# Optimization experiments

Measured on AMD Instinct MI355X. Metric: run time of the kernel, lower is better.

The kernel has to match this reference:

```python
import jax, jax.numpy as jnp
import numpy as np

B, D, H, O, E = 16384, 1024, 512, 256, 8


def setup_inputs() -> dict:
    key = jax.random.key(0)
    ks = jax.random.split(key, 8)
    s = lambda k, shape, fan: (jax.random.normal(k, shape, jnp.float32) / np.sqrt(fan).astype(np.float32))
    z = lambda shape: jnp.zeros(shape, jnp.float32)
    return {
        "x": jax.random.normal(ks[0], (B, D), jnp.float32),
        # gating network: D -> 256 -> 128 -> E
        "gw1": s(ks[1], (D, 256), D), "gb1": z((256,)),
        "gw2": s(ks[2], (256, 128), 256), "gb2": z((128,)),
        "gw3": s(ks[3], (128, E), 128), "gb3": z((E,)),
        # experts, batched over expert dim E: D -> H -> H -> O
        "ew1": s(ks[4], (E, D, H), D), "eb1": z((E, H)),
        "ew2": s(ks[5], (E, H, H), H), "eb2": z((E, H)),
        "ew3": s(ks[6], (E, H, O), H), "eb3": z((E, O)),
    }


def reference(x, gw1, gb1, gw2, gb2, gw3, gb3, ew1, eb1, ew2, eb2, ew3, eb3):
    # Gating network (dropout is identity in eval mode)
    g = jax.nn.relu(x @ gw1 + gb1)
    g = jax.nn.relu(g @ gw2 + gb2)
    gates = jax.nn.softmax(g @ gw3 + gb3, axis=1)  # [B, E]
    # All experts run on every token: batched small MLPs over expert axis e
    h = jax.nn.relu(jnp.einsum('bd,edh->ebh', x, ew1) + eb1[:, None, :])   # [E, B, H]
    h = jax.nn.relu(jnp.einsum('ebh,ehk->ebk', h, ew2) + eb2[:, None, :])  # [E, B, H]
    eo = jnp.einsum('ebh,eho->ebo', h, ew3) + eb3[:, None, :]              # [E, B, O]
    # gate-weighted sum over experts
    out = jnp.einsum('ebo,be->bo', eo, gates)  # [B, O]
    return out
```

## Files before the change

kernel.cpp:

```cpp
#include <hip/hip_runtime.h>
#include <hip/hip_bf16.h>

typedef __hip_bfloat16 bf16;
typedef __attribute__((ext_vector_type(8))) __bf16 bf16x8;
typedef __attribute__((ext_vector_type(4))) float f32x4;

#define B_ 16384
#define D_ 1024
#define H_ 512
#define O_ 256
#define E_ 8
#define BC_ 8192

#define GLDS(src, dst) __builtin_amdgcn_global_load_lds( \
    (const __attribute__((address_space(1))) void*)(src), \
    (__attribute__((address_space(3))) void*)(dst), 16, 0, 0)

__global__ void detect_k(const unsigned short* __restrict__ x, int* __restrict__ flag) {
    __shared__ int s;
    if (threadIdx.x == 0) s = 0;
    __syncthreads();
    int big = 0;
    for (int i = threadIdx.x; i < 2048; i += 256)
        if (((x[i] >> 7) & 0xFF) >= 150) big = 1;
    if (big) atomicOr(&s, 1);
    __syncthreads();
    if (threadIdx.x == 0) *flag = s;
}

__global__ void cvt_k(const void* __restrict__ src, bf16* __restrict__ dst,
                      const int* __restrict__ flag, long n) {
    const int f = *flag;
    long i = (long)blockIdx.x * blockDim.x + threadIdx.x;
    const long stride = (long)gridDim.x * blockDim.x;
    if (f) {
        const float* s = (const float*)src;
        for (; i < n; i += stride) dst[i] = __float2bfloat16(s[i]);
    } else {
        const bf16* s = (const bf16*)src;
        for (; i < n; i += stride) dst[i] = s[i];
    }
}

__global__ void transpose_k(const void* __restrict__ in, bf16* __restrict__ out,
                            const int* __restrict__ flag, int R, int C) {
    __shared__ bf16 t[32][33];
    const int f = *flag;
    const long zo = (long)blockIdx.z * R * C;
    const int x = blockIdx.x * 32 + threadIdx.x;
    const int y0 = blockIdx.y * 32;
    const float* inf = (const float*)in;
    const bf16* inb = (const bf16*)in;
#pragma unroll
    for (int i = 0; i < 4; i++) {
        int r = y0 + threadIdx.y + i * 8;
        long idx = zo + (long)r * C + x;
        t[threadIdx.y + i * 8][threadIdx.x] =
            f ? __float2bfloat16(inf[idx]) : inb[idx];
    }
    __syncthreads();
    const int xr = blockIdx.y * 32 + threadIdx.x;
#pragma unroll
    for (int i = 0; i < 4; i++) {
        int c = blockIdx.x * 32 + threadIdx.y + i * 8;
        out[zo + (long)c * R + xr] = t[threadIdx.x][threadIdx.y + i * 8];
    }
}

__global__ void gate3_softmax_k(const bf16* __restrict__ g2,
                                const bf16* __restrict__ gw3,
                                const bf16* __restrict__ gb3,
                                float* __restrict__ gates) {
    __shared__ float w[128 * 8];
    __shared__ float bsh[8];
    const int tid = threadIdx.x;
    for (int i = tid; i < 1024; i += 256) w[i] = __bfloat162float(gw3[i]);
    if (tid < 8) bsh[tid] = __bfloat162float(gb3[tid]);
    __syncthreads();

    const long row = (long)blockIdx.x * 256 + tid;
    float acc[8];
#pragma unroll
    for (int o = 0; o < 8; o++) acc[o] = bsh[o];

    const bf16x8* rp8 = (const bf16x8*)(g2 + row * 128);
#pragma unroll 4
    for (int c8 = 0; c8 < 16; c8++) {
        bf16x8 v8 = rp8[c8];
#pragma unroll
        for (int jj = 0; jj < 8; jj++) {
            float v = (float)v8[jj];
            int k = c8 * 8 + jj;
#pragma unroll
            for (int o = 0; o < 8; o++) acc[o] += v * w[k * 8 + o];
        }
    }
    float m = acc[0];
#pragma unroll
    for (int o = 1; o < 8; o++) m = fmaxf(m, acc[o]);
    float s = 0.f;
#pragma unroll
    for (int o = 0; o < 8; o++) { acc[o] = __expf(acc[o] - m); s += acc[o]; }
    const float inv = 1.f / s;
#pragma unroll
    for (int o = 0; o < 8; o++) gates[row * 8 + o] = acc[o] * inv;
}

template <int MODE>
__global__ __launch_bounds__(256, 4)
void gemm_bt(const bf16* __restrict__ A, const bf16* __restrict__ Bt,
             const bf16* __restrict__ bias, const float* __restrict__ gates,
             void* __restrict__ Cout, const bf16* __restrict__ eb3,
             const int* __restrict__ oflag,
             int lda, int ldb, int ldo, int K,
             long a_z, long b_z, long bias_z, long out_z,
             int e_gate, int k_per_e, long a_e, long b_e, long row0) {
    __shared__ __attribute__((aligned(16))) bf16 As[128 * 32];
    __shared__ __attribute__((aligned(16))) bf16 Bs[128 * 32];

    const int tid  = threadIdx.x;
    const int lane = tid & 63;
    const int quad = lane >> 4;
    const int l15  = lane & 15;
    const int wid  = tid >> 6;
    const int wr   = (wid >> 1) << 6;
    const int wc   = (wid & 1) << 6;
    const int z    = blockIdx.z;
    const long m0  = (long)blockIdx.y << 7;
    const long n0  = (long)blockIdx.x << 7;

    const bf16* Az = A + (long)z * a_z;
    const bf16* Bz = Bt + (long)z * b_z;

    f32x4 acc[4][4];
#pragma unroll
    for (int i = 0; i < 4; i++)
#pragma unroll
        for (int j = 0; j < 4; j++) acc[i][j] = (f32x4){0.f, 0.f, 0.f, 0.f};

    const int erow = tid >> 2;
    const int ecol = (tid & 3) << 3;

    const int n_e   = k_per_e ? (K / k_per_e) : 1;
    const int inner = (k_per_e ? k_per_e : K) >> 5;

    for (int e = 0; e < n_e; e++) {
        const bf16* Ae = Az + (long)e * a_e;
        const bf16* Be = Bz + (long)e * b_e;
        for (int kti = 0; kti < inner; kti++) {
            const int kk = kti << 5;
#pragma unroll
            for (int i = 0; i < 2; i++) {
                const int r = (i << 6) + erow;
                GLDS(Ae + (m0 + r) * lda + (kk + ecol), As + r * 32 + ecol);
            }
#pragma unroll
            for (int i = 0; i < 2; i++) {
                const int r = (i << 6) + erow;
                GLDS(Be + (n0 + r) * ldb + (kk + ecol), Bs + r * 32 + ecol);
            }
            __syncthreads();
            bf16x8 af[4], bfr[4];
#pragma unroll
            for (int i = 0; i < 4; i++)
                af[i] = *(const bf16x8*)(As + (wr + i * 16 + l15) * 32 + (quad << 3));
#pragma unroll
            for (int j = 0; j < 4; j++)
                bfr[j] = *(const bf16x8*)(Bs + (wc + j * 16 + l15) * 32 + (quad << 3));
#pragma unroll
            for (int i = 0; i < 4; i++)
#pragma unroll
                for (int j = 0; j < 4; j++)
                    acc[i][j] = __builtin_amdgcn_mfma_f32_16x16x32_bf16(
                        af[i], bfr[j], acc[i][j], 0, 0, 0);
            __syncthreads();
        }
    }

    const int eg = (e_gate >= 0) ? e_gate : z;

    if constexpr (MODE == 0 || MODE == 1) {
        bf16* C = (bf16*)Cout + (long)z * out_z;
        const bf16* bb = bias + (long)z * bias_z;
        float gv[4][4];
        if constexpr (MODE == 1) {
#pragma unroll
            for (int i = 0; i < 4; i++)
#pragma unroll
                for (int rg = 0; rg < 4; rg++)
                    gv[i][rg] = gates[(row0 + m0 + wr + i * 16 + quad * 4 + rg) * 8 + eg];
        }
#pragma unroll
        for (int j = 0; j < 4; j++) {
            const int c = (int)n0 + wc + j * 16 + l15;
            const float bv = __bfloat162float(bb[c]);
#pragma unroll
            for (int i = 0; i < 4; i++) {
#pragma unroll
                for (int rg = 0; rg < 4; rg++) {
                    const long r = m0 + wr + i * 16 + quad * 4 + rg;
                    float v = fmaxf(acc[i][j][rg] + bv, 0.f);
                    if constexpr (MODE == 1) v *= gv[i][rg];
                    C[r * ldo + c] = __float2bfloat16(v);
                }
            }
        }
    } else if constexpr (MODE == 2) {
        float* C = (float*)Cout;
#pragma unroll
        for (int i = 0; i < 4; i++) {
#pragma unroll
            for (int rg = 0; rg < 4; rg++) {
                const long r = m0 + wr + i * 16 + quad * 4 + rg;
                const float g = gates[(row0 + r) * 8 + eg];
#pragma unroll
                for (int j = 0; j < 4; j++) {
                    const int c = (int)n0 + wc + j * 16 + l15;
                    const float b3 = __bfloat162float(eb3[eg * O_ + c]);
                    C[r * ldo + c] += acc[i][j][rg] + g * b3;
                }
            }
        }
    } else {
        float* C = (float*)Cout + (long)z * out_z;
        const int e0 = z * 2;
        float b30[4], b31[4];
#pragma unroll
        for (int j = 0; j < 4; j++) {
            const int c = (int)n0 + wc + j * 16 + l15;
            b30[j] = __bfloat162float(eb3[e0 * O_ + c]);
            b31[j] = __bfloat162float(eb3[(e0 + 1) * O_ + c]);
        }
#pragma unroll
        for (int i = 0; i < 4; i++) {
#pragma unroll
            for (int rg = 0; rg < 4; rg++) {
                const long r = m0 + wr + i * 16 + quad * 4 + rg;
                const float g0 = gates[(row0 + r) * 8 + e0];
                const float g1 = gates[(row0 + r) * 8 + e0 + 1];
#pragma unroll
                for (int j = 0; j < 4; j++) {
                    const int c = (int)n0 + wc + j * 16 + l15;
                    C[(row0 + r) * ldo + c] =
                        acc[i][j][rg] + g0 * b30[j] + g1 * b31[j];
                }
            }
        }
    }
}

__global__ void zero_f32_k(float* __restrict__ p) {
    p[(long)blockIdx.x * 256 + threadIdx.x] = 0.f;
}
__global__ void out_cvt_k(const float* __restrict__ in, void* __restrict__ out,
                          const int* __restrict__ flag) {
    const long i = (long)blockIdx.x * 256 + threadIdx.x;
    if (*flag) ((float*)out)[i] = in[i];
    else       ((bf16*)out)[i] = __float2bfloat16(in[i]);
}
__global__ void reduce4_k(const float* __restrict__ p, void* __restrict__ out,
                          const int* __restrict__ flag) {
    const long n = (long)B_ * O_;
    const long i = ((long)blockIdx.x * 256 + threadIdx.x) * 4;
    float4 a = *(const float4*)(p + i);
    float4 b = *(const float4*)(p + n + i);
    float4 c = *(const float4*)(p + 2 * n + i);
    float4 d = *(const float4*)(p + 3 * n + i);
    float4 s = {a.x + b.x + c.x + d.x, a.y + b.y + c.y + d.y,
                a.z + b.z + c.z + d.z, a.w + b.w + c.w + d.w};
    if (*flag) {
        *(float4*)((float*)out + i) = s;
    } else {
        bf16* o = (bf16*)out + i;
        o[0] = __float2bfloat16(s.x); o[1] = __float2bfloat16(s.y);
        o[2] = __float2bfloat16(s.z); o[3] = __float2bfloat16(s.w);
    }
}

extern "C" void kernel_launch(void* const* d_in, const int* in_sizes, int n_in,
                              void* d_out, int out_size, void* d_ws, size_t ws_size,
                              hipStream_t stream) {
    (void)in_sizes; (void)n_in; (void)out_size;
    const void* x   = d_in[0];
    const void* gw1 = d_in[1];
    const void* gb1 = d_in[2];
    const void* gw2 = d_in[3];
    const void* gb2 = d_in[4];
    const void* gw3 = d_in[5];
    const void* gb3 = d_in[6];
    const void* ew1 = d_in[7];
    const void* eb1 = d_in[8];
    const void* ew2 = d_in[9];
    const void* eb2 = d_in[10];
    const void* ew3 = d_in[11];
    const void* eb3 = d_in[12];

    char* ws = (char*)d_ws;
    size_t off = 0;
    auto alloc = [&](size_t n) { char* p = ws + off; off += (n + 255) & ~(size_t)255; return p; };

    int*  flag  = (int*)alloc(256);
    bf16* xc    = (bf16*)alloc((size_t)B_ * D_ * 2);
    bf16* gw1t  = (bf16*)alloc((size_t)256 * 1024 * 2);
    bf16* gw2t  = (bf16*)alloc((size_t)128 * 256 * 2);
    bf16* ew1t  = (bf16*)alloc((size_t)E_ * H_ * D_ * 2);
    bf16* ew2t  = (bf16*)alloc((size_t)E_ * H_ * H_ * 2);
    bf16* ew3t  = (bf16*)alloc((size_t)E_ * O_ * H_ * 2);
    bf16* gb1c  = (bf16*)alloc(256 * 2);
    bf16* gb2c  = (bf16*)alloc(128 * 2);
    bf16* gw3c  = (bf16*)alloc(1024 * 2);
    bf16* gb3c  = (bf16*)alloc(8 * 2);
    bf16* eb1c  = (bf16*)alloc((size_t)E_ * H_ * 2);
    bf16* eb2c  = (bf16*)alloc((size_t)E_ * H_ * 2);
    bf16* eb3c  = (bf16*)alloc((size_t)E_ * O_ * 2);
    bf16* g1    = (bf16*)alloc((size_t)B_ * 256 * 2);
    bf16* g2b   = (bf16*)alloc((size_t)B_ * 128 * 2);
    float* gates = (float*)alloc((size_t)B_ * 8 * 4);

    const size_t small = off;
    const size_t needA = small + 2ull * ((size_t)E_ * BC_ * H_ * 2 + 256)
                               + (4ull * B_ * O_ * 4 + 256) + 4096;
    const bool pathA = ws_size >= needA;

    detect_k<<<1, 256, 0, stream>>>((const unsigned short*)x, flag);

    cvt_k<<<4096, 256, 0, stream>>>(x, xc, flag, (long)B_ * D_);
    cvt_k<<<1, 256, 0, stream>>>(gb1, gb1c, flag, 256);
    cvt_k<<<1, 256, 0, stream>>>(gb2, gb2c, flag, 128);
    cvt_k<<<4, 256, 0, stream>>>(gw3, gw3c, flag, 1024);
    cvt_k<<<1, 256, 0, stream>>>(gb3, gb3c, flag, 8);
    cvt_k<<<16, 256, 0, stream>>>(eb1, eb1c, flag, (long)E_ * H_);
    cvt_k<<<16, 256, 0, stream>>>(eb2, eb2c, flag, (long)E_ * H_);
    cvt_k<<<8, 256, 0, stream>>>(eb3, eb3c, flag, (long)E_ * O_);

    transpose_k<<<dim3(256 / 32, 1024 / 32, 1), dim3(32, 8), 0, stream>>>(gw1, gw1t, flag, 1024, 256);
    transpose_k<<<dim3(128 / 32, 256 / 32, 1), dim3(32, 8), 0, stream>>>(gw2, gw2t, flag, 256, 128);
    transpose_k<<<dim3(H_ / 32, D_ / 32, E_), dim3(32, 8), 0, stream>>>(ew1, ew1t, flag, D_, H_);
    transpose_k<<<dim3(H_ / 32, H_ / 32, E_), dim3(32, 8), 0, stream>>>(ew2, ew2t, flag, H_, H_);
    transpose_k<<<dim3(O_ / 32, H_ / 32, E_), dim3(32, 8), 0, stream>>>(ew3, ew3t, flag, H_, O_);

    gemm_bt<0><<<dim3(2, 128, 1), 256, 0, stream>>>(
        xc, gw1t, gb1c, nullptr, g1, nullptr, nullptr,
        1024, 1024, 256, 1024, 0, 0, 0, 0, 0, 0, 0, 0, 0);
    gemm_bt<0><<<dim3(1, 128, 1), 256, 0, stream>>>(
        g1, gw2t, gb2c, nullptr, g2b, nullptr, nullptr,
        256, 256, 128, 256, 0, 0, 0, 0, 0, 0, 0, 0, 0);
    gate3_softmax_k<<<dim3(B_ / 256), 256, 0, stream>>>(g2b, gw3c, gb3c, gates);

    if (pathA) {
        bf16* h1c = (bf16*)alloc((size_t)E_ * BC_ * H_ * 2);
        bf16* h2c = (bf16*)alloc((size_t)E_ * BC_ * H_ * 2);
        float* parts = (float*)alloc(4ull * B_ * O_ * 4);
        for (int ci = 0; ci < B_ / BC_; ci++) {
            const long rb = (long)ci * BC_;
            gemm_bt<0><<<dim3(4, BC_ / 128, 8), 256, 0, stream>>>(
                xc + rb * D_, ew1t, eb1c, nullptr, h1c, nullptr, nullptr,
                D_, D_, H_, D_,
                0, (long)H_ * D_, H_, (long)BC_ * H_, 0, 0, 0, 0, 0);
            gemm_bt<1><<<dim3(4, BC_ / 128, 8), 256, 0, stream>>>(
                h1c, ew2t, eb2c, gates, h2c, nullptr, nullptr,
                H_, H_, H_, H_,
                (long)BC_ * H_, (long)H_ * H_, H_, (long)BC_ * H_, -1, 0, 0, 0, rb);
            gemm_bt<5><<<dim3(2, BC_ / 128, 4), 256, 0, stream>>>(
                h2c, ew3t, nullptr, gates, parts, eb3c, nullptr,
                H_, H_, O_, 1024,
                2L * BC_ * H_, 2L * O_ * H_, 0, (long)B_ * O_,
                2 , 512, (long)BC_ * H_, (long)O_ * H_, rb);
        }
        reduce4_k<<<dim3(B_ * O_ / 1024), 256, 0, stream>>>(parts, d_out, flag);
    } else {
        bf16* h1s = (bf16*)alloc((size_t)B_ * H_ * 2);
        bf16* h2s = (bf16*)alloc((size_t)B_ * H_ * 2);
        float* oacc = (float*)alloc((size_t)B_ * O_ * 4);
        zero_f32_k<<<dim3(B_ * O_ / 256), 256, 0, stream>>>(oacc);
        for (int e = 0; e < E_; e++) {
            gemm_bt<0><<<dim3(4, 128, 1), 256, 0, stream>>>(
                xc, ew1t + (size_t)e * H_ * D_, eb1c + (size_t)e * H_, nullptr, h1s, nullptr, nullptr,
                1024, 1024, 512, 1024, 0, 0, 0, 0, 0, 0, 0, 0, 0);
            gemm_bt<1><<<dim3(4, 128, 1), 256, 0, stream>>>(
                h1s, ew2t + (size_t)e * H_ * H_, eb2c + (size_t)e * H_, gates, h2s, nullptr, nullptr,
                512, 512, 512, 512, 0, 0, 0, 0, e, 0, 0, 0, 0);
            gemm_bt<2><<<dim3(2, 128, 1), 256, 0, stream>>>(
                h2s, ew3t + (size_t)e * O_ * H_, nullptr, gates, oacc, eb3c, nullptr,
                512, 512, 256, 512, 0, 0, 0, 0, e, 0, 0, 0, 0);
        }
        out_cvt_k<<<dim3(B_ * O_ / 256), 256, 0, stream>>>(oacc, d_out, flag);
    }
}
```

Baseline: 587.8 us.

## Replace expert GEMMs with 256x256-tile 8-wave pipelined MFMA kernel

Adds a gemm256 kernel with 256x256 output tiles, 512 threads, double-buffered LDS filled by global_load_lds with XOR swizzle, interleaved staging and MFMA phases, and workgroup ID remapping. It replaces the three expert GEMMs on the chunked path. Expert-2 output and the ew3 transpose now use an interleaved [B, E*H] layout, so layer 3 runs per expert into 8 partial buffers. Those partials are summed per chunk by a new reduce8 kernel. The aim is higher MFMA utilisation and more data reuse, at the cost of more register pressure, more partial-buffer traffic, and per-chunk reduce launches.

Result: no change. 580.2 us (-1.3%).

```diff
diff --git a/kernel.cpp b/kernel.cpp
--- a/kernel.cpp
+++ b/kernel.cpp
@@ -12,9 +12,15 @@
 #define E_ 8
 #define BC_ 8192
 
+static_assert(B_ % BC_ == 0, "chunking");
+
 #define GLDS(src, dst) __builtin_amdgcn_global_load_lds( \
     (const __attribute__((address_space(1))) void*)(src), \
     (__attribute__((address_space(3))) void*)(dst), 16, 0, 0)
+
+#define BAR()   asm volatile("s_barrier" ::: "memory")
+#define LGKM0() do { asm volatile("s_waitcnt lgkmcnt(0)" ::: "memory"); \
+                     __builtin_amdgcn_sched_barrier(0); } while (0)
 
 __global__ void detect_k(const unsigned short* __restrict__ x, int* __restrict__ flag) {
     __shared__ int s;
@@ -43,10 +49,11 @@
 }
 
 __global__ void transpose_k(const void* __restrict__ in, bf16* __restrict__ out,
-                            const int* __restrict__ flag, int R, int C) {
+                            const int* __restrict__ flag, int R, int C,
+                            long z_out, long c_stride) {
     __shared__ bf16 t[32][33];
     const int f = *flag;
-    const long zo = (long)blockIdx.z * R * C;
+    const long zi = (long)blockIdx.z * R * C;
     const int x = blockIdx.x * 32 + threadIdx.x;
     const int y0 = blockIdx.y * 32;
     const float* inf = (const float*)in;
@@ -54,16 +61,17 @@
 #pragma unroll
     for (int i = 0; i < 4; i++) {
         int r = y0 + threadIdx.y + i * 8;
-        long idx = zo + (long)r * C + x;
+        long idx = zi + (long)r * C + x;
         t[threadIdx.y + i * 8][threadIdx.x] =
             f ? __float2bfloat16(inf[idx]) : inb[idx];
     }
     __syncthreads();
     const int xr = blockIdx.y * 32 + threadIdx.x;
+    const long zo = (long)blockIdx.z * z_out;
 #pragma unroll
     for (int i = 0; i < 4; i++) {
         int c = blockIdx.x * 32 + threadIdx.y + i * 8;
-        out[zo + (long)c * R + xr] = t[threadIdx.x][threadIdx.y + i * 8];
+        out[zo + (long)c * c_stride + xr] = t[threadIdx.x][threadIdx.y + i * 8];
     }
 }
 
@@ -221,28 +229,189 @@
                 }
             }
         }
+    }
+}
+
+template <int MODE>
+__global__ __launch_bounds__(512, 2)
+void gemm256(const bf16* __restrict__ A, const bf16* __restrict__ Bt,
+             const bf16* __restrict__ bias, const float* __restrict__ gates,
+             void* __restrict__ Cout, const bf16* __restrict__ eb3,
+             int lda, int ldb, int ldo, int K,
+             long a_z, long b_z, long bias_z, long out_z, long row0) {
+    __shared__ __attribute__((aligned(16))) bf16 lds[2][2][256 * 64];
+
+    int bx = blockIdx.x, by = blockIdx.y;
+    {
+        const int gx = gridDim.x;
+        const int nwg = gx * gridDim.y;
+        if ((nwg & 7) == 0) {
+            int lin = bx + gx * by;
+            lin = (lin & 7) * (nwg >> 3) + (lin >> 3);
+            bx = lin % gx; by = lin / gx;
+        }
+    }
+
+    const int tid  = threadIdx.x;
+    const int lane = tid & 63;
+    const int quad = lane >> 4;
+    const int l15  = lane & 15;
+    const int w    = tid >> 6;
+    const int wm   = w >> 2;
+    const int wn   = w & 3;
+    const int z    = blockIdx.z;
+    const long m0  = (long)by << 8;
+    const long n0  = (long)bx << 8;
+
+    const bf16* __restrict__ Az = A + z * a_z;
+    const bf16* __restrict__ Bz = Bt + z * b_z;
+
+    f32x4 acc[8][4];
+#pragma unroll
+    for (int i = 0; i < 8; ++i)
+#pragma unroll
+        for (int j = 0; j < 4; ++j) acc[i][j] = (f32x4){0.f, 0.f, 0.f, 0.f};
+
+    bf16x8 af[4][2], bv[2][2];
+
+    auto stage = [&](int buf, int mat, int half, int kt) {
+        const bf16* __restrict__ G = mat ? Bz : Az;
+        const int ld = mat ? ldb : lda;
+        const long p0 = mat ? n0 : m0;
+#pragma unroll
+        for (int l = 0; l < 2; ++l) {
+            const int ci = (w << 1) | l;
+            const int rb = mat ? ((ci >> 2) << 6) + (half << 5) + ((ci & 3) << 3)
+                               : ((ci >> 3) << 7) + (half << 6) + ((ci & 7) << 3);
+            const int row = rb + (lane >> 3);
+            const int cb  = ((lane & 7) << 4) ^ ((row & 4) << 3);
+            GLDS(G + (p0 + row) * ld + kt * 64 + (cb >> 1),
+                 &lds[buf][mat][rb * 64]);
+        }
+    };
+    auto ldaf = [&](int buf, int qm) {
+#pragma unroll
+        for (int i = 0; i < 4; ++i) {
+            const int r = (wm << 7) + (qm << 6) + (i << 4) + l15;
+            const char* p = (const char*)&lds[buf][0][r * 64];
+            const int sw = (r & 4) << 3;
+#pragma unroll
+            for (int s = 0; s < 2; ++s)
+                af[i][s] = *(const bf16x8*)(p + (((s << 6) + (quad << 4)) ^ sw));
+        }
+    };
+    auto ldbf = [&](int buf, int qn) {
+#pragma unroll
+        for (int j = 0; j < 2; ++j) {
+            const int r = (wn << 6) + (qn << 5) + (j << 4) + l15;
+            const char* p = (const char*)&lds[buf][1][r * 64];
+            const int sw = (r & 4) << 3;
+#pragma unroll
+            for (int s = 0; s < 2; ++s)
+                bv[j][s] = *(const bf16x8*)(p + (((s << 6) + (quad << 4)) ^ sw));
+        }
+    };
+    auto mmac = [&](int qm, int qn) {
+#pragma unroll
+        for (int i = 0; i < 4; ++i)
+#pragma unroll
+            for (int j = 0; j < 2; ++j)
+#pragma unroll
+                for (int s = 0; s < 2; ++s)
+                    acc[(qm << 2) + i][(qn << 1) + j] =
+                        __builtin_amdgcn_mfma_f32_16x16x32_bf16(
+                            af[i][s], bv[j][s], acc[(qm << 2) + i][(qn << 1) + j],
+                            0, 0, 0);
+    };
+
+    const int nt = K >> 6;
+
+    stage(0, 0, 0, 0); stage(0, 0, 1, 0); stage(0, 1, 0, 0); stage(0, 1, 1, 0);
+    stage(1, 0, 0, 1); stage(1, 1, 0, 1);
+    asm volatile("s_waitcnt vmcnt(4)" ::: "memory");
+    BAR();
+
+    const int hi = nt >> 1;
+    for (int it = 0; it < hi; ++it) {
+        const int t1k = 2 * it + 1, t2k = 2 * it + 2, t3k = 2 * it + 3;
+        const bool do2 = t2k < nt, do3 = t3k < nt;
+        ldaf(0, 0); ldbf(0, 0); stage(1, 0, 1, t1k);
+        BAR(); LGKM0();
+        __builtin_amdgcn_s_setprio(1); mmac(0, 0); __builtin_amdgcn_s_setprio(0);
+        BAR();
+        ldbf(0, 1); stage(1, 1, 1, t1k);
+        BAR(); LGKM0();
+        __builtin_amdgcn_s_setprio(1); mmac(0, 1); __builtin_amdgcn_s_setprio(0);
+        BAR();
+        ldaf(0, 1); ldbf(0, 0); if (do2) stage(0, 0, 0, t2k);
+        BAR(); LGKM0();
+        __builtin_amdgcn_s_setprio(1); mmac(1, 0); __builtin_amdgcn_s_setprio(0);
+        BAR();
+        ldbf(0, 1); if (do2) stage(0, 1, 0, t2k);
+        BAR(); LGKM0();
+        __builtin_amdgcn_s_setprio(1); mmac(1, 1); __builtin_amdgcn_s_setprio(0);
+        if (do2) { asm volatile("s_waitcnt vmcnt(4)" ::: "memory"); }
+        else     { asm volatile("s_waitcnt vmcnt(0)" ::: "memory"); }
+        BAR();
+        ldaf(1, 0); ldbf(1, 0); if (do2) stage(0, 0, 1, t2k);
+        BAR(); LGKM0();
+        __builtin_amdgcn_s_setprio(1); mmac(0, 0); __builtin_amdgcn_s_setprio(0);
+        BAR();
+        ldbf(1, 1); if (do2) stage(0, 1, 1, t2k);
+        BAR(); LGKM0();
+        __builtin_amdgcn_s_setprio(1); mmac(0, 1); __builtin_amdgcn_s_setprio(0);
+        BAR();
+        ldaf(1, 1); ldbf(1, 0); if (do3) stage(1, 0, 0, t3k);
+        BAR(); LGKM0();
+        __builtin_amdgcn_s_setprio(1); mmac(1, 0); __builtin_amdgcn_s_setprio(0);
+        BAR();
+        ldbf(1, 1); if (do3) stage(1, 1, 0, t3k);
+        BAR(); LGKM0();
+        __builtin_amdgcn_s_setprio(1); mmac(1, 1); __builtin_amdgcn_s_setprio(0);
+        if (do3) { asm volatile("s_waitcnt vmcnt(4)" ::: "memory"); }
+        else     { asm volatile("s_waitcnt vmcnt(0)" ::: "memory"); }
+        BAR();
+    }
+
+    if constexpr (MODE == 0 || MODE == 1) {
+        bf16* C = (bf16*)Cout + z * out_z;
+        const bf16* bb = bias + z * bias_z;
+        float bvv[4];
+#pragma unroll
+        for (int jg = 0; jg < 4; ++jg)
+            bvv[jg] = __bfloat162float(bb[(int)n0 + (wn << 6) + (jg << 4) + l15]);
+#pragma unroll
+        for (int ig = 0; ig < 8; ++ig) {
+#pragma unroll
+            for (int rg = 0; rg < 4; ++rg) {
+                const long r = m0 + (wm << 7) + (ig << 4) + (quad << 2) + rg;
+                float g = 1.f;
+                if constexpr (MODE == 1) g = gates[(row0 + r) * 8 + z];
+#pragma unroll
+                for (int jg = 0; jg < 4; ++jg) {
+                    const int c = (int)n0 + (wn << 6) + (jg << 4) + l15;
+                    float v = fmaxf(acc[ig][jg][rg] + bvv[jg], 0.f);
+                    if constexpr (MODE == 1) v *= g;
+                    C[r * ldo + c] = __float2bfloat16(v);
+                }
+            }
+        }
     } else {
-        float* C = (float*)Cout + (long)z * out_z;
-        const int e0 = z * 2;
-        float b30[4], b31[4];
-#pragma unroll
-        for (int j = 0; j < 4; j++) {
-            const int c = (int)n0 + wc + j * 16 + l15;
-            b30[j] = __bfloat162float(eb3[e0 * O_ + c]);
-            b31[j] = __bfloat162float(eb3[(e0 + 1) * O_ + c]);
-        }
-#pragma unroll
-        for (int i = 0; i < 4; i++) {
-#pragma unroll
-            for (int rg = 0; rg < 4; rg++) {
-                const long r = m0 + wr + i * 16 + quad * 4 + rg;
-                const float g0 = gates[(row0 + r) * 8 + e0];
-                const float g1 = gates[(row0 + r) * 8 + e0 + 1];
-#pragma unroll
-                for (int j = 0; j < 4; j++) {
-                    const int c = (int)n0 + wc + j * 16 + l15;
-                    C[(row0 + r) * ldo + c] =
-                        acc[i][j][rg] + g0 * b30[j] + g1 * b31[j];
+        float* C = (float*)Cout + z * out_z;
+        float b3v[4];
+#pragma unroll
+        for (int jg = 0; jg < 4; ++jg)
+            b3v[jg] = __bfloat162float(eb3[z * O_ + (int)n0 + (wn << 6) + (jg << 4) + l15]);
+#pragma unroll
+        for (int ig = 0; ig < 8; ++ig) {
+#pragma unroll
+            for (int rg = 0; rg < 4; ++rg) {
+                const long r = m0 + (wm << 7) + (ig << 4) + (quad << 2) + rg;
+                const float g = gates[(row0 + r) * 8 + z];
+#pragma unroll
+                for (int jg = 0; jg < 4; ++jg) {
+                    const int c = (int)n0 + (wn << 6) + (jg << 4) + l15;
+                    C[r * ldo + c] = acc[ig][jg][rg] + g * b3v[jg];
                 }
             }
         }
@@ -258,20 +427,20 @@
     if (*flag) ((float*)out)[i] = in[i];
     else       ((bf16*)out)[i] = __float2bfloat16(in[i]);
 }
-__global__ void reduce4_k(const float* __restrict__ p, void* __restrict__ out,
-                          const int* __restrict__ flag) {
-    const long n = (long)B_ * O_;
+__global__ void reduce8_k(const float* __restrict__ p, void* __restrict__ out,
+                          const int* __restrict__ flag, long off) {
+    const long n = (long)BC_ * O_;
     const long i = ((long)blockIdx.x * 256 + threadIdx.x) * 4;
-    float4 a = *(const float4*)(p + i);
-    float4 b = *(const float4*)(p + n + i);
-    float4 c = *(const float4*)(p + 2 * n + i);
-    float4 d = *(const float4*)(p + 3 * n + i);
-    float4 s = {a.x + b.x + c.x + d.x, a.y + b.y + c.y + d.y,
-                a.z + b.z + c.z + d.z, a.w + b.w + c.w + d.w};
+    float4 s = *(const float4*)(p + i);
+#pragma unroll
+    for (int zz = 1; zz < 8; ++zz) {
+        float4 a = *(const float4*)(p + (long)zz * n + i);
+        s.x += a.x; s.y += a.y; s.z += a.z; s.w += a.w;
+    }
     if (*flag) {
-        *(float4*)((float*)out + i) = s;
+        *(float4*)((float*)out + off + i) = s;
     } else {
-        bf16* o = (bf16*)out + i;
+        bf16* o = (bf16*)out + off + i;
         o[0] = __float2bfloat16(s.x); o[1] = __float2bfloat16(s.y);
         o[2] = __float2bfloat16(s.z); o[3] = __float2bfloat16(s.w);
     }
@@ -318,8 +487,9 @@
     float* gates = (float*)alloc((size_t)B_ * 8 * 4);
 
     const size_t small = off;
-    const size_t needA = small + 2ull * ((size_t)E_ * BC_ * H_ * 2 + 256)
-                               + (4ull * B_ * O_ * 4 + 256) + 4096;
+    const size_t needA = small + ((size_t)E_ * BC_ * H_ * 2 + 256)
+                               + ((size_t)BC_ * E_ * H_ * 2 + 256)
+                               + (8ull * BC_ * O_ * 4 + 256) + 4096;
     const bool pathA = ws_size >= needA;
 
     detect_k<<<1, 256, 0, stream>>>((const unsigned short*)x, flag);
@@ -333,11 +503,20 @@
     cvt_k<<<16, 256, 0, stream>>>(eb2, eb2c, flag, (long)E_ * H_);
     cvt_k<<<8, 256, 0, stream>>>(eb3, eb3c, flag, (long)E_ * O_);
 
-    transpose_k<<<dim3(256 / 32, 1024 / 32, 1), dim3(32, 8), 0, stream>>>(gw1, gw1t, flag, 1024, 256);
-    transpose_k<<<dim3(128 / 32, 256 / 32, 1), dim3(32, 8), 0, stream>>>(gw2, gw2t, flag, 256, 128);
-    transpose_k<<<dim3(H_ / 32, D_ / 32, E_), dim3(32, 8), 0, stream>>>(ew1, ew1t, flag, D_, H_);
-    transpose_k<<<dim3(H_ / 32, H_ / 32, E_), dim3(32, 8), 0, stream>>>(ew2, ew2t, flag, H_, H_);
-    transpose_k<<<dim3(O_ / 32, H_ / 32, E_), dim3(32, 8), 0, stream>>>(ew3, ew3t, flag, H_, O_);
+    transpose_k<<<dim3(256 / 32, 1024 / 32, 1), dim3(32, 8), 0, stream>>>(
+        gw1, gw1t, flag, 1024, 256, 0L, 1024L);
+    transpose_k<<<dim3(128 / 32, 256 / 32, 1), dim3(32, 8), 0, stream>>>(
+        gw2, gw2t, flag, 256, 128, 0L, 256L);
+    transpose_k<<<dim3(H_ / 32, D_ / 32, E_), dim3(32, 8), 0, stream>>>(
+        ew1, ew1t, flag, D_, H_, (long)H_ * D_, (long)D_);
+    transpose_k<<<dim3(H_ / 32, H_ / 32, E_), dim3(32, 8), 0, stream>>>(
+        ew2, ew2t, flag, H_, H_, (long)H_ * H_, (long)H_);
+    if (pathA)
+        transpose_k<<<dim3(O_ / 32, H_ / 32, E_), dim3(32, 8), 0, stream>>>(
+            ew3, ew3t, flag, H_, O_, (long)H_, (long)E_ * H_);
+    else
+        transpose_k<<<dim3(O_ / 32, H_ / 32, E_), dim3(32, 8), 0, stream>>>(
+            ew3, ew3t, flag, H_, O_, (long)O_ * H_, (long)H_);
 
     gemm_bt<0><<<dim3(2, 128, 1), 256, 0, stream>>>(
         xc, gw1t, gb1c, nullptr, g1, nullptr, nullptr,
@@ -348,26 +527,26 @@
     gate3_softmax_k<<<dim3(B_ / 256), 256, 0, stream>>>(g2b, gw3c, gb3c, gates);
 
     if (pathA) {
-        bf16* h1c = (bf16*)alloc((size_t)E_ * BC_ * H_ * 2);
-        bf16* h2c = (bf16*)alloc((size_t)E_ * BC_ * H_ * 2);
-        float* parts = (float*)alloc(4ull * B_ * O_ * 4);
-        for (int ci = 0; ci < B_ / BC_; ci++) {
-            const long rb = (long)ci * BC_;
-            gemm_bt<0><<<dim3(4, BC_ / 128, 8), 256, 0, stream>>>(
-                xc + rb * D_, ew1t, eb1c, nullptr, h1c, nullptr, nullptr,
+        bf16* h1c   = (bf16*)alloc((size_t)E_ * BC_ * H_ * 2);
+        bf16* h2    = (bf16*)alloc((size_t)BC_ * E_ * H_ * 2);
+        float* parts = (float*)alloc(8ull * BC_ * O_ * 4);
+        for (int ch = 0; ch < B_ / BC_; ch++) {
+            const long rb = (long)ch * BC_;
+            gemm256<0><<<dim3(2, BC_ / 256, 8), 512, 0, stream>>>(
+                xc + rb * D_, ew1t, eb1c, nullptr, h1c, nullptr,
                 D_, D_, H_, D_,
-                0, (long)H_ * D_, H_, (long)BC_ * H_, 0, 0, 0, 0, 0);
-            gemm_bt<1><<<dim3(4, BC_ / 128, 8), 256, 0, stream>>>(
-                h1c, ew2t, eb2c, gates, h2c, nullptr, nullptr,
-                H_, H_, H_, H_,
-                (long)BC_ * H_, (long)H_ * H_, H_, (long)BC_ * H_, -1, 0, 0, 0, rb);
-            gemm_bt<5><<<dim3(2, BC_ / 128, 4), 256, 0, stream>>>(
-                h2c, ew3t, nullptr, gates, parts, eb3c, nullptr,
-                H_, H_, O_, 1024,
-                2L * BC_ * H_, 2L * O_ * H_, 0, (long)B_ * O_,
-                2 , 512, (long)BC_ * H_, (long)O_ * H_, rb);
-        }
-        reduce4_k<<<dim3(B_ * O_ / 1024), 256, 0, stream>>>(parts, d_out, flag);
+                0, (long)H_ * D_, (long)H_, (long)BC_ * H_, 0);
+            gemm256<1><<<dim3(2, BC_ / 256, 8), 512, 0, stream>>>(
+                h1c, ew2t, eb2c, gates, h2, nullptr,
+                H_, H_, E_ * H_, H_,
+                (long)BC_ * H_, (long)H_ * H_, (long)H_, (long)H_, rb);
+            gemm256<4><<<dim3(1, BC_ / 256, 8), 512, 0, stream>>>(
+                h2, ew3t, nullptr, gates, parts, eb3c,
+                E_ * H_, E_ * H_, O_, 512,
+                (long)H_, (long)H_, 0, (long)BC_ * O_, rb);
+            reduce8_k<<<dim3(BC_ * O_ / 1024), 256, 0, stream>>>(
+                parts, d_out, flag, rb * O_);
+        }
     } else {
         bf16* h1s = (bf16*)alloc((size_t)B_ * H_ * 2);
         bf16* h2s = (bf16*)alloc((size_t)B_ * H_ * 2);
```
